# Kernel tuning notes

Measured on AMD Instinct MI355X. Metric: run time of the kernel, lower is better.

Reference implementation:

```python
import jax, jax.numpy as jnp
import numpy as np
import math

B, N = 16, 32            # batch, num_agents
D_OBS = 128              # obs_input_dim
N_ACT = 16               # num_actions
D_OA_IN = D_OBS + N_ACT  # obs_act_input_dim = 144
D_OUT = 128              # obs_output_dim == obs_act_output_dim
HID = 64                 # final hidden
FINAL_OUT = 1


def _xavier(k, shape):
    fan_out, fan_in = shape
    lim = math.sqrt(6.0 / (fan_in + fan_out))
    return jax.random.uniform(k, shape, jnp.float32, -lim, lim)


def setup_inputs() -> dict:
    key = jax.random.key(0)
    ks = jax.random.split(key, 12)
    return {
        "states": jax.random.normal(ks[0], (B, N, D_OBS), jnp.float32),
        "policies": jax.random.uniform(ks[1], (B, N, N_ACT), jnp.float32),
        "actions": jax.random.uniform(ks[2], (B, N, N_ACT), jnp.float32),
        # uniform noise in [0,1); forward applies (noise-0.5)*0.1 like torch.rand path
        "noise": jax.random.uniform(ks[3], (B, N, N, N, D_OUT), jnp.float32),
        # torch Linear weights: [out_features, in_features], bias=False
        "Wk_oa": _xavier(ks[4], (D_OUT, D_OA_IN)),
        "Wq_oa": _xavier(ks[5], (D_OUT, D_OA_IN)),
        "Wv_oa": _xavier(ks[6], (D_OUT, D_OA_IN)),
        "Wk_o": _xavier(ks[7], (D_OUT, D_OBS)),
        "Wq_o": _xavier(ks[8], (D_OUT, D_OBS)),
        "Wv_o": _xavier(ks[9], (D_OUT, D_OBS)),
        "W1": _xavier(ks[10], (HID, 2 * D_OUT)),
        "W2": _xavier(ks[11], (FINAL_OUT, HID)),
    }


def reference(states, policies, actions, noise, Wk_oa, Wq_oa, Wv_oa, Wk_o, Wq_o, Wv_o, W1, W2):
    n = states.shape[1]
    d_oa = Wk_oa.shape[0]
    d_o = Wk_o.shape[0]

    obs_actions = jnp.concatenate([states, actions], axis=-1)   # [B,N,D_oa_in]
    obs_policy = jnp.concatenate([states, policies], axis=-1)

    # --- obs-action attention branch ---
    K = obs_actions @ Wk_oa.T                                   # [B,N,d]
    Q = obs_actions @ Wq_oa.T
    # bmm(Q,K^T).transpose(1,2): score_t[b,j,i] = Q_i . K_j; softmax over i
    score_t = jnp.einsum('bid,bjd->bji', Q, K)
    w_oa = jax.nn.softmax(score_t / jnp.sqrt(jnp.asarray(d_oa, states.dtype)), axis=-1)  # [B,N,N]

    # place_policies/place_actions: diagonal picks obs_policy, off-diag obs_actions
    eye = jnp.eye(n, dtype=states.dtype)[None, :, :, None]       # [1,N,N,1]
    oap = eye * obs_policy[:, None, :, :] + (1.0 - eye) * obs_actions[:, None, :, :]  # [B,N,N,D_oa_in]
    AV = oap @ Wv_oa.T                                           # [B,N,N,d]

    # mean_i( AV[b,j,i,:] * w_oa[b,k,i] + (noise-0.5)*0.1 ); mean is linear -> split
    noise_mean = jnp.mean((noise - 0.5) * 0.1, axis=-2)          # [B,N,N,d]
    wav = jnp.einsum('bjid,bki->bkjd', AV, w_oa) / n + noise_mean  # [B,N,N,d]

    # --- obs-only attention branch ---
    Ko = states @ Wk_o.T
    Qo = states @ Wq_o.T
    AVO = states @ Wv_o.T                                        # [B,N,d]
    score_o = jnp.einsum('bid,bjd->bji', Qo, Ko)
    w_o = jax.nn.softmax(score_o / jnp.sqrt(jnp.asarray(d_o, states.dtype)), axis=-1)  # [B,N,N]
    wfo = jnp.einsum('bji,bid->bjd', w_o, AVO) / n               # [B,N,d]
    wfo_b = jnp.broadcast_to(wfo[:, :, None, :], wav.shape[:3] + (d_o,))  # [B,N,N,d]

    node = jnp.concatenate([wfo_b, wav], axis=-1)                # [B,N,N,2d]
    h = jax.nn.leaky_relu(node @ W1.T, negative_slope=0.01)
    value = h @ W2.T                                             # [B,N,N,1]
    return (value, w_oa, w_o[..., None])
```

## Files before the change

kernel.cpp:

```cpp
#include <hip/hip_runtime.h>


#define WS_K    0
#define WS_Q    65536
#define WS_VA   131072
#define WS_KO   196608
#define WS_QO   262144
#define WS_AVO  327680
#define WS_SDIV 393216
#define WS_DDIV 458752
#define WS_U    524288
#define WS_WOA  557056

__global__ __launch_bounds__(256) void k_transforms(
    const float* __restrict__ states, const float* __restrict__ policies,
    const float* __restrict__ actions,
    const float* __restrict__ Wk_oa, const float* __restrict__ Wq_oa,
    const float* __restrict__ Wv_oa, const float* __restrict__ Wk_o,
    const float* __restrict__ Wq_o,  const float* __restrict__ Wv_o,
    float* __restrict__ ws)
{
    __shared__ __align__(16) float xa[144];
    const int row = blockIdx.x;
    const int t = threadIdx.x;
    if (t < 128)       xa[t] = states[row * 128 + t];
    else if (t < 144)  xa[t] = actions[row * 16 + (t - 128)];
    __syncthreads();

    for (int u = t; u < 768; u += 256) {
        const int m = u >> 7, o = u & 127;
        const float* Wrow; int len4; float* dst;
        switch (m) {
            case 0: Wrow = Wk_oa + o * 144; len4 = 36; dst = ws + WS_K;  break;
            case 1: Wrow = Wq_oa + o * 144; len4 = 36; dst = ws + WS_Q;  break;
            case 2: Wrow = Wv_oa + o * 144; len4 = 36; dst = ws + WS_VA; break;
            case 3: Wrow = Wk_o  + o * 128; len4 = 32; dst = ws + WS_KO; break;
            case 4: Wrow = Wq_o  + o * 128; len4 = 32; dst = ws + WS_QO; break;
            default:Wrow = Wv_o  + o * 128; len4 = 32; dst = ws + WS_AVO;break;
        }
        const float4* W4 = (const float4*)Wrow;
        const float4* x4 = (const float4*)xa;
        float acc = 0.f;
        for (int c = 0; c < len4; ++c) {
            float4 w = W4[c], x = x4[c];
            acc += w.x * x.x + w.y * x.y + w.z * x.z + w.w * x.w;
        }
        dst[row * 128 + o] = acc;
    }
}

__global__ __launch_bounds__(256) void k_attn(
    const float* __restrict__ policies, const float* __restrict__ actions,
    const float* __restrict__ Wv_oa, const float* __restrict__ W1,
    float* __restrict__ ws, float* __restrict__ out)
{
    const float* K   = ws + WS_K;
    const float* Q   = ws + WS_Q;
    const float* Va  = ws + WS_VA;
    const float* Ko  = ws + WS_KO;
    const float* Qo  = ws + WS_QO;
    const float* AVO = ws + WS_AVO;
    float* Sdiv = ws + WS_SDIV;
    float* Ddiv = ws + WS_DDIV;
    float* U    = ws + WS_U;
    float* Woa  = ws + WS_WOA;

    const int b = blockIdx.x >> 5, r = blockIdx.x & 31;
    const int t = threadIdx.x;
    const int br = b * 32 + r;

    __shared__ __align__(16) float kr[128], kor[128], wfo[128];
    __shared__ float sA[32], sO[32], woa[32], wo[32], pd[16];

    if (t < 32) out[br * 32 + t] = 0.f;
    if (t < 128) { kr[t] = K[br * 128 + t]; kor[t] = Ko[br * 128 + t]; }
    else if (t < 144) {
        int c = t - 128;
        pd[c] = policies[br * 16 + c] - actions[br * 16 + c];
    }
    __syncthreads();

    {
        const int i = t >> 3, seg = t & 7;
        const float4* q4  = (const float4*)(Q  + (b * 32 + i) * 128) + seg * 4;
        const float4* qo4 = (const float4*)(Qo + (b * 32 + i) * 128) + seg * 4;
        const float4* k4  = (const float4*)kr  + seg * 4;
        const float4* ko4 = (const float4*)kor + seg * 4;
        float a0 = 0.f, a1 = 0.f;
        #pragma unroll
        for (int c = 0; c < 4; ++c) {
            float4 q = q4[c], kk = k4[c];
            a0 += q.x * kk.x + q.y * kk.y + q.z * kk.z + q.w * kk.w;
            float4 p = qo4[c], mm = ko4[c];
            a1 += p.x * mm.x + p.y * mm.y + p.z * mm.z + p.w * mm.w;
        }
        #pragma unroll
        for (int off = 1; off < 8; off <<= 1) {
            a0 += __shfl_xor(a0, off, 64);
            a1 += __shfl_xor(a1, off, 64);
        }
        if (seg == 0) {
            const float scale = 0.08838834764831845f;
            sA[i] = a0 * scale;
            sO[i] = a1 * scale;
        }
    }
    __syncthreads();

    if (t < 64) {
        const int i = t & 31;
        float s = (t < 32) ? sA[i] : sO[i];
        float m = s;
        #pragma unroll
        for (int off = 1; off < 32; off <<= 1) m = fmaxf(m, __shfl_xor(m, off, 64));
        float e = __expf(s - m);
        float sum = e;
        #pragma unroll
        for (int off = 1; off < 32; off <<= 1) sum += __shfl_xor(sum, off, 64);
        float w = e / sum;
        if (t < 32) { woa[i] = w; out[16384 + br * 32 + i] = w; Woa[br * 32 + i] = w; }
        else        { wo[i]  = w; out[32768 + br * 32 + i] = w; }
    }
    __syncthreads();

    {
        const int d = t & 127;
        const float* M  = (t < 128) ? Va  : AVO;
        const float* wp = (t < 128) ? woa : wo;
        float acc = 0.f;
        #pragma unroll 8
        for (int i = 0; i < 32; ++i) acc += wp[i] * M[(b * 32 + i) * 128 + d];
        if (t < 128) {
            Sdiv[br * 128 + d] = acc * (1.f / 32.f);
            const float4* wv4 = (const float4*)(Wv_oa + d * 144 + 128);
            float dv = 0.f;
            #pragma unroll
            for (int c = 0; c < 4; ++c) {
                float4 w = wv4[c];
                dv += w.x * pd[4*c] + w.y * pd[4*c+1] + w.z * pd[4*c+2] + w.w * pd[4*c+3];
            }
            Ddiv[br * 128 + d] = dv * (1.f / 32.f);
        } else {
            wfo[d] = acc * (1.f / 32.f);
        }
    }
    __syncthreads();

    {
        const int h = t >> 2, qq = t & 3;
        const float4* w4 = (const float4*)(W1 + h * 256) + qq * 8;
        const float4* f4 = (const float4*)wfo + qq * 8;
        float acc = 0.f;
        #pragma unroll
        for (int c = 0; c < 8; ++c) {
            float4 w = w4[c], f = f4[c];
            acc += w.x * f.x + w.y * f.y + w.z * f.z + w.w * f.w;
        }
        acc += __shfl_xor(acc, 1, 64);
        acc += __shfl_xor(acc, 2, 64);
        if (qq == 0) U[br * 64 + h] = acc;
    }
}

__global__ __launch_bounds__(256) void k_value(
    const float* __restrict__ noise, const float* __restrict__ ws,
    const float* __restrict__ W1, const float* __restrict__ W2,
    float* __restrict__ out)
{
    const float* Sdiv = ws + WS_SDIV;
    const float* Ddiv = ws + WS_DDIV;
    const float* U    = ws + WS_U;
    const float* Woa  = ws + WS_WOA;

    const int blk = blockIdx.x;
    const int b  = blk >> 6;
    const int k  = (blk >> 1) & 31;
    const int j0 = (blk & 1) * 16;
    const int t  = threadIdx.x;
    const int l  = t & 63, wv = t >> 6;
    const int h  = t >> 2, q = t & 3;
    const int bk = b * 32 + k;

    __shared__ __align__(16) float wavs[2][4][36];
    __shared__ __align__(16) float sdiv_s[128];
    __shared__ __align__(16) float ddiv_s[16 * 128];
    __shared__ float woa_s[16];

    float w1r[32];
    {
        const float4* p = (const float4*)(W1 + h * 256 + 128 + q * 32);
        #pragma unroll
        for (int c = 0; c < 8; ++c) {
            float4 v = p[c];
            w1r[4*c] = v.x; w1r[4*c+1] = v.y; w1r[4*c+2] = v.z; w1r[4*c+3] = v.w;
        }
    }
    const float u_h  = U[bk * 64 + h];
    const float w2_h = W2[h];

    if (t < 32) ((float4*)sdiv_s)[t] = ((const float4*)(Sdiv + bk * 128))[t];
    {
        const float4* dsrc = (const float4*)(Ddiv + (b * 32 + j0) * 128);
        ((float4*)ddiv_s)[t]       = dsrc[t];
        ((float4*)ddiv_s)[t + 256] = dsrc[t + 256];
    }
    if (t < 16) woa_s[t] = Woa[bk * 32 + j0 + t];
    __syncthreads();

    const int d4 = (wv << 3) + (l & 7);
    const int i0 = l >> 3;
    const float4* nb = (const float4*)noise + (size_t)bk * 32768 + (size_t)(i0 * 32 + d4);

    float4 n0, n1, n2, n3;
    {
        const float4* p = nb + (size_t)j0 * 1024;
        n0 = p[0]; n1 = p[256]; n2 = p[512]; n3 = p[768];
    }
    #pragma unroll 2
    for (int jj = 0; jj < 16; ++jj) {
        const int j = j0 + jj;
        float4 m0{}, m1{}, m2{}, m3{};
        if (jj < 15) {
            const float4* p = nb + (size_t)(j + 1) * 1024;
            m0 = p[0]; m1 = p[256]; m2 = p[512]; m3 = p[768];
        }
        float sx = n0.x + n1.x + n2.x + n3.x;
        float sy = n0.y + n1.y + n2.y + n3.y;
        float sz = n0.z + n1.z + n2.z + n3.z;
        float sw = n0.w + n1.w + n2.w + n3.w;
        #pragma unroll
        for (int off = 8; off < 64; off <<= 1) {
            sx += __shfl_xor(sx, off, 64);
            sy += __shfl_xor(sy, off, 64);
            sz += __shfl_xor(sz, off, 64);
            sw += __shfl_xor(sw, off, 64);
        }
        const float woaj = woa_s[jj];
        if (l < 8) {
            const int db = (wv << 5) + (l << 2);
            float4 w;
            w.x = sdiv_s[db+0] + ddiv_s[jj*128+db+0] * woaj + sx * (0.1f/32.f) - 0.05f;
            w.y = sdiv_s[db+1] + ddiv_s[jj*128+db+1] * woaj + sy * (0.1f/32.f) - 0.05f;
            w.z = sdiv_s[db+2] + ddiv_s[jj*128+db+2] * woaj + sz * (0.1f/32.f) - 0.05f;
            w.w = sdiv_s[db+3] + ddiv_s[jj*128+db+3] * woaj + sw * (0.1f/32.f) - 0.05f;
            *(float4*)&wavs[jj & 1][wv][l << 2] = w;
        }
        asm volatile("s_waitcnt lgkmcnt(0)" ::: "memory");
        __builtin_amdgcn_s_barrier();
        __builtin_amdgcn_sched_barrier(0);
        {
            const float4* w4 = (const float4*)&wavs[jj & 1][q][0];
            float acc = 0.f;
            #pragma unroll
            for (int c = 0; c < 8; ++c) {
                float4 v = w4[c];
                acc += w1r[4*c] * v.x + w1r[4*c+1] * v.y
                     + w1r[4*c+2] * v.z + w1r[4*c+3] * v.w;
            }
            acc += __shfl_xor(acc, 1, 64);
            acc += __shfl_xor(acc, 2, 64);
            float vp = 0.f;
            if (q == 0) {
                float hv = u_h + acc;
                hv = (hv > 0.f) ? hv : 0.01f * hv;
                vp = hv * w2_h;
            }
            #pragma unroll
            for (int off = 4; off < 64; off <<= 1) vp += __shfl_xor(vp, off, 64);
            if (l == 0) atomicAdd(out + bk * 32 + j, vp);
        }
        n0 = m0; n1 = m1; n2 = m2; n3 = m3;
    }
}

extern "C" void kernel_launch(void* const* d_in, const int* in_sizes, int n_in,
                              void* d_out, int out_size, void* d_ws, size_t ws_size,
                              hipStream_t stream) {
    const float* states   = (const float*)d_in[0];
    const float* policies = (const float*)d_in[1];
    const float* actions  = (const float*)d_in[2];
    const float* noise    = (const float*)d_in[3];
    const float* Wk_oa    = (const float*)d_in[4];
    const float* Wq_oa    = (const float*)d_in[5];
    const float* Wv_oa    = (const float*)d_in[6];
    const float* Wk_o     = (const float*)d_in[7];
    const float* Wq_o     = (const float*)d_in[8];
    const float* Wv_o     = (const float*)d_in[9];
    const float* W1       = (const float*)d_in[10];
    const float* W2       = (const float*)d_in[11];
    float* out = (float*)d_out;
    float* ws  = (float*)d_ws;

    k_transforms<<<512, 256, 0, stream>>>(states, policies, actions,
                                          Wk_oa, Wq_oa, Wv_oa, Wk_o, Wq_o, Wv_o, ws);
    k_attn<<<512, 256, 0, stream>>>(policies, actions, Wv_oa, W1, ws, out);
    k_value<<<1024, 256, 0, stream>>>(noise, ws, W1, W2, out);
}
```

Baseline: 417.1 us.

## Move noise reduction into front kernel alongside projections; simplify value kernel

The noise mean reduction, which streams the 128 MB noise tensor, moves out of the value kernel into the first kernel as extra blocks that run alongside the projection blocks. The reduced sums go to a workspace buffer. The value kernel then reads those sums plus Ddiv, uses one block per (b,k), and writes outputs directly instead of using atomics, so the zeroing of out in the attention kernel is dropped. The aim is to overlap the bandwidth-bound noise pass with the small projection work and shorten the serial chain, at the cost of an extra workspace round trip and two block barriers per j in the value kernel.

```diff
diff --git a/kernel.cpp b/kernel.cpp
--- a/kernel.cpp
+++ b/kernel.cpp
@@ -11,41 +11,87 @@
 #define WS_DDIV 458752
 #define WS_U    524288
 #define WS_WOA  557056
-
-__global__ __launch_bounds__(256) void k_transforms(
+#define WS_NS   573440
+
+__global__ __launch_bounds__(256) void k_front(
     const float* __restrict__ states, const float* __restrict__ policies,
     const float* __restrict__ actions,
     const float* __restrict__ Wk_oa, const float* __restrict__ Wq_oa,
     const float* __restrict__ Wv_oa, const float* __restrict__ Wk_o,
     const float* __restrict__ Wq_o,  const float* __restrict__ Wv_o,
-    float* __restrict__ ws)
+    const float* __restrict__ noise, float* __restrict__ ws)
 {
-    __shared__ __align__(16) float xa[144];
-    const int row = blockIdx.x;
     const int t = threadIdx.x;
-    if (t < 128)       xa[t] = states[row * 128 + t];
-    else if (t < 144)  xa[t] = actions[row * 16 + (t - 128)];
-    __syncthreads();
-
-    for (int u = t; u < 768; u += 256) {
-        const int m = u >> 7, o = u & 127;
-        const float* Wrow; int len4; float* dst;
-        switch (m) {
-            case 0: Wrow = Wk_oa + o * 144; len4 = 36; dst = ws + WS_K;  break;
-            case 1: Wrow = Wq_oa + o * 144; len4 = 36; dst = ws + WS_Q;  break;
-            case 2: Wrow = Wv_oa + o * 144; len4 = 36; dst = ws + WS_VA; break;
-            case 3: Wrow = Wk_o  + o * 128; len4 = 32; dst = ws + WS_KO; break;
-            case 4: Wrow = Wq_o  + o * 128; len4 = 32; dst = ws + WS_QO; break;
-            default:Wrow = Wv_o  + o * 128; len4 = 32; dst = ws + WS_AVO;break;
-        }
-        const float4* W4 = (const float4*)Wrow;
-        const float4* x4 = (const float4*)xa;
-        float acc = 0.f;
-        for (int c = 0; c < len4; ++c) {
-            float4 w = W4[c], x = x4[c];
-            acc += w.x * x.x + w.y * x.y + w.z * x.z + w.w * x.w;
-        }
-        dst[row * 128 + o] = acc;
+    if (blockIdx.x < 512) {
+        __shared__ __align__(16) float xa[144];
+        const int row = blockIdx.x;
+        if (t < 128)       xa[t] = states[row * 128 + t];
+        else if (t < 144)  xa[t] = actions[row * 16 + (t - 128)];
+        __syncthreads();
+
+        for (int u = t; u < 768; u += 256) {
+            const int m = u >> 7, o = u & 127;
+            const float* Wrow; int len4; float* dst;
+            switch (m) {
+                case 0: Wrow = Wk_oa + o * 144; len4 = 36; dst = ws + WS_K;  break;
+                case 1: Wrow = Wq_oa + o * 144; len4 = 36; dst = ws + WS_Q;  break;
+                case 2: Wrow = Wv_oa + o * 144; len4 = 36; dst = ws + WS_VA; break;
+                case 3: Wrow = Wk_o  + o * 128; len4 = 32; dst = ws + WS_KO; break;
+                case 4: Wrow = Wq_o  + o * 128; len4 = 32; dst = ws + WS_QO; break;
+                default:Wrow = Wv_o  + o * 128; len4 = 32; dst = ws + WS_AVO;break;
+            }
+            const float4* W4 = (const float4*)Wrow;
+            const float4* x4 = (const float4*)xa;
+            float acc = 0.f;
+            for (int c = 0; c < len4; ++c) {
+                float4 w = W4[c], x = x4[c];
+                acc += w.x * x.x + w.y * x.y + w.z * x.z + w.w * x.w;
+            }
+            dst[row * 128 + o] = acc;
+        }
+    } else {
+        const int blk = blockIdx.x - 512;
+        const int b  = blk >> 6;
+        const int k  = (blk >> 1) & 31;
+        const int j0 = (blk & 1) * 16;
+        const int l  = t & 63, wv = t >> 6;
+        const int bk = b * 32 + k;
+
+        const int d4 = (wv << 3) + (l & 7);
+        const int i0 = l >> 3;
+        const float4* nb = (const float4*)noise + (size_t)bk * 32768
+                         + (size_t)(i0 * 32 + d4);
+        float4* ns4 = (float4*)(ws + WS_NS);
+
+        float4 n0, n1, n2, n3;
+        {
+            const float4* p = nb + (size_t)j0 * 1024;
+            n0 = p[0]; n1 = p[256]; n2 = p[512]; n3 = p[768];
+        }
+        for (int jj = 0; jj < 16; ++jj) {
+            const int j = j0 + jj;
+            float4 m0{}, m1{}, m2{}, m3{};
+            if (jj < 15) {
+                const float4* p = nb + (size_t)(j + 1) * 1024;
+                m0 = p[0]; m1 = p[256]; m2 = p[512]; m3 = p[768];
+            }
+            float sx = n0.x + n1.x + n2.x + n3.x;
+            float sy = n0.y + n1.y + n2.y + n3.y;
+            float sz = n0.z + n1.z + n2.z + n3.z;
+            float sw = n0.w + n1.w + n2.w + n3.w;
+            #pragma unroll
+            for (int off = 8; off < 64; off <<= 1) {
+                sx += __shfl_xor(sx, off, 64);
+                sy += __shfl_xor(sy, off, 64);
+                sz += __shfl_xor(sz, off, 64);
+                sw += __shfl_xor(sw, off, 64);
+            }
+            if (l < 8) {
+                float4 v; v.x = sx; v.y = sy; v.z = sz; v.w = sw;
+                ns4[(size_t)(bk * 32 + j) * 32 + (wv << 3) + l] = v;
+            }
+            n0 = m0; n1 = m1; n2 = m2; n3 = m3;
+        }
     }
 }
 
@@ -72,7 +118,6 @@
     __shared__ __align__(16) float kr[128], kor[128], wfo[128];
     __shared__ float sA[32], sO[32], woa[32], wo[32], pd[16];
 
-    if (t < 32) out[br * 32 + t] = 0.f;
     if (t < 128) { kr[t] = K[br * 128 + t]; kor[t] = Ko[br * 128 + t]; }
     else if (t < 144) {
         int c = t - 128;
@@ -163,28 +208,25 @@
 }
 
 __global__ __launch_bounds__(256) void k_value(
-    const float* __restrict__ noise, const float* __restrict__ ws,
-    const float* __restrict__ W1, const float* __restrict__ W2,
-    float* __restrict__ out)
+    const float* __restrict__ ws, const float* __restrict__ W1,
+    const float* __restrict__ W2, float* __restrict__ out)
 {
     const float* Sdiv = ws + WS_SDIV;
     const float* Ddiv = ws + WS_DDIV;
     const float* U    = ws + WS_U;
     const float* Woa  = ws + WS_WOA;
-
-    const int blk = blockIdx.x;
-    const int b  = blk >> 6;
-    const int k  = (blk >> 1) & 31;
-    const int j0 = (blk & 1) * 16;
+    const float* NS   = ws + WS_NS;
+
+    const int bk = blockIdx.x;
+    const int b  = bk >> 5;
     const int t  = threadIdx.x;
+    const int h  = t >> 2, q = t & 3;
     const int l  = t & 63, wv = t >> 6;
-    const int h  = t >> 2, q = t & 3;
-    const int bk = b * 32 + k;
-
-    __shared__ __align__(16) float wavs[2][4][36];
+
+    __shared__ __align__(16) float wav_s[2][4][36];
     __shared__ __align__(16) float sdiv_s[128];
-    __shared__ __align__(16) float ddiv_s[16 * 128];
-    __shared__ float woa_s[16];
+    __shared__ float woa_s[32];
+    __shared__ float wsum[2][4];
 
     float w1r[32];
     {
@@ -197,59 +239,27 @@
     }
     const float u_h  = U[bk * 64 + h];
     const float w2_h = W2[h];
-
     if (t < 32) ((float4*)sdiv_s)[t] = ((const float4*)(Sdiv + bk * 128))[t];
-    {
-        const float4* dsrc = (const float4*)(Ddiv + (b * 32 + j0) * 128);
-        ((float4*)ddiv_s)[t]       = dsrc[t];
-        ((float4*)ddiv_s)[t + 256] = dsrc[t + 256];
-    }
-    if (t < 16) woa_s[t] = Woa[bk * 32 + j0 + t];
-    __syncthreads();
-
-    const int d4 = (wv << 3) + (l & 7);
-    const int i0 = l >> 3;
-    const float4* nb = (const float4*)noise + (size_t)bk * 32768 + (size_t)(i0 * 32 + d4);
-
-    float4 n0, n1, n2, n3;
-    {
-        const float4* p = nb + (size_t)j0 * 1024;
-        n0 = p[0]; n1 = p[256]; n2 = p[512]; n3 = p[768];
-    }
-    #pragma unroll 2
-    for (int jj = 0; jj < 16; ++jj) {
-        const int j = j0 + jj;
-        float4 m0{}, m1{}, m2{}, m3{};
-        if (jj < 15) {
-            const float4* p = nb + (size_t)(j + 1) * 1024;
-            m0 = p[0]; m1 = p[256]; m2 = p[512]; m3 = p[768];
-        }
-        float sx = n0.x + n1.x + n2.x + n3.x;
-        float sy = n0.y + n1.y + n2.y + n3.y;
-        float sz = n0.z + n1.z + n2.z + n3.z;
-        float sw = n0.w + n1.w + n2.w + n3.w;
-        #pragma unroll
-        for (int off = 8; off < 64; off <<= 1) {
-            sx += __shfl_xor(sx, off, 64);
-            sy += __shfl_xor(sy, off, 64);
-            sz += __shfl_xor(sz, off, 64);
-            sw += __shfl_xor(sw, off, 64);
-        }
-        const float woaj = woa_s[jj];
-        if (l < 8) {
-            const int db = (wv << 5) + (l << 2);
-            float4 w;
-            w.x = sdiv_s[db+0] + ddiv_s[jj*128+db+0] * woaj + sx * (0.1f/32.f) - 0.05f;
-            w.y = sdiv_s[db+1] + ddiv_s[jj*128+db+1] * woaj + sy * (0.1f/32.f) - 0.05f;
-            w.z = sdiv_s[db+2] + ddiv_s[jj*128+db+2] * woaj + sz * (0.1f/32.f) - 0.05f;
-            w.w = sdiv_s[db+3] + ddiv_s[jj*128+db+3] * woaj + sw * (0.1f/32.f) - 0.05f;
-            *(float4*)&wavs[jj & 1][wv][l << 2] = w;
-        }
-        asm volatile("s_waitcnt lgkmcnt(0)" ::: "memory");
-        __builtin_amdgcn_s_barrier();
-        __builtin_amdgcn_sched_barrier(0);
+    if (t >= 32 && t < 64) woa_s[t - 32] = Woa[bk * 32 + (t - 32)];
+    __syncthreads();
+
+    float dv = 0.f, nv = 0.f;
+    if (t < 128) {
+        dv = Ddiv[(b * 32) * 128 + t];
+        nv = NS[(size_t)(bk * 32) * 128 + t];
+    }
+    for (int j = 0; j < 32; ++j) {
+        float dvn = 0.f, nvn = 0.f;
+        if (j < 31 && t < 128) {
+            dvn = Ddiv[(b * 32 + j + 1) * 128 + t];
+            nvn = NS[(size_t)(bk * 32 + j + 1) * 128 + t];
+        }
+        if (t < 128)
+            wav_s[j & 1][t >> 5][t & 31] =
+                sdiv_s[t] + dv * woa_s[j] + nv * (0.1f / 32.f) - 0.05f;
+        __syncthreads();
         {
-            const float4* w4 = (const float4*)&wavs[jj & 1][q][0];
+            const float4* w4 = (const float4*)&wav_s[j & 1][q][0];
             float acc = 0.f;
             #pragma unroll
             for (int c = 0; c < 8; ++c) {
@@ -267,9 +277,13 @@
             }
             #pragma unroll
             for (int off = 4; off < 64; off <<= 1) vp += __shfl_xor(vp, off, 64);
-            if (l == 0) atomicAdd(out + bk * 32 + j, vp);
-        }
-        n0 = m0; n1 = m1; n2 = m2; n3 = m3;
+            if (l == 0) wsum[j & 1][wv] = vp;
+        }
+        __syncthreads();
+        if (t == 0)
+            out[bk * 32 + j] = wsum[j & 1][0] + wsum[j & 1][1]
+                             + wsum[j & 1][2] + wsum[j & 1][3];
+        dv = dvn; nv = nvn;
     }
 }
 
@@ -291,8 +305,9 @@
     float* out = (float*)d_out;
     float* ws  = (float*)d_ws;
 
-    k_transforms<<<512, 256, 0, stream>>>(states, policies, actions,
-                                          Wk_oa, Wq_oa, Wv_oa, Wk_o, Wq_o, Wv_o, ws);
+    k_front<<<1536, 256, 0, stream>>>(states, policies, actions,
+                                      Wk_oa, Wq_oa, Wv_oa, Wk_o, Wq_o, Wv_o,
+                                      noise, ws);
     k_attn<<<512, 256, 0, stream>>>(policies, actions, Wv_oa, W1, ws, out);
-    k_value<<<1024, 256, 0, stream>>>(noise, ws, W1, W2, out);
+    k_value<<<512, 256, 0, stream>>>(ws, W1, W2, out);
 }
```

New measurement: 435.6 us. +4.4%, slower.
